# Kernel optimization log

Measured on AMD Instinct MI355X. Metric: run time of the kernel, lower is better.

Reference implementation:

```python
import jax, jax.numpy as jnp
import numpy as np

POOLED_SIZES = [12, 16, 20, 24]
NUM_HEADS = 8
EPS_LN = 1e-5


def _pool_mat(in_size, out_size):
    # torch adaptive_avg_pool1d/2d semantics as an averaging matrix [out, in]
    m = np.zeros((out_size, in_size), np.float32)
    for i in range(out_size):
        s = (i * in_size) // out_size
        e = -((-(i + 1) * in_size) // out_size)  # ceil
        m[i, s:e] = 1.0 / (e - s)
    return jnp.asarray(m)


def _dwconv(x, w, b):
    # depthwise 3x3, stride 1, padding 1 (NCHW, OIHW with I=1)
    y = jax.lax.conv_general_dilated(
        x, w, (1, 1), 'SAME', feature_group_count=x.shape[1],
        dimension_numbers=('NCHW', 'OIHW', 'NCHW'))
    return y + b[None, :, None, None]


def _ln(x, g, b):
    m = x.mean(-1, keepdims=True)
    v = jnp.mean((x - m) ** 2, axis=-1, keepdims=True)
    return (x - m) / jnp.sqrt(v + EPS_LN) * g + b


def setup_inputs() -> dict:
    key = jax.random.key(0)
    ks = jax.random.split(key, 16)
    B, H, W, C = 4, 56, 56, 256
    hid = 4 * C
    nrm = lambda k, shape, s=0.02: jax.random.normal(k, shape, jnp.float32) * s
    inp = {
        'x': jax.random.normal(ks[0], (B, H * W, C), jnp.float32),
        'cpe_w': nrm(ks[1], (C, 1, 3, 3)), 'cpe_b': jnp.zeros((C,), jnp.float32),
        'norm1_w': jnp.ones((C,), jnp.float32), 'norm1_b': jnp.zeros((C,), jnp.float32),
        'q_w': nrm(ks[2], (C, C)),
        'kv_w': nrm(ks[3], (2 * C, C)),
        'attn_norm_w': jnp.ones((C,), jnp.float32), 'attn_norm_b': jnp.zeros((C,), jnp.float32),
        'proj_w': nrm(ks[4], (C, C)), 'proj_b': jnp.zeros((C,), jnp.float32),
        'norm2_w': jnp.ones((C,), jnp.float32), 'norm2_b': jnp.zeros((C,), jnp.float32),
        'fc1_w': nrm(ks[5], (hid, C)), 'fc1_b': jnp.zeros((hid,), jnp.float32),
        'irb_conv_w': nrm(ks[6], (hid, 1, 3, 3)), 'irb_conv_b': jnp.zeros((hid,), jnp.float32),
        'fc2_w': nrm(ks[7], (C, hid)), 'fc2_b': jnp.zeros((C,), jnp.float32),
        'H': H, 'W': W,
    }
    for i in range(4):
        inp[f'dconv{i}_w'] = nrm(ks[8 + i], (C, 1, 3, 3))
        inp[f'dconv{i}_b'] = jnp.zeros((C,), jnp.float32)
    return inp


def _forward(x, cpe_w, cpe_b, norm1_w, norm1_b, q_w, kv_w, attn_norm_w, attn_norm_b,
             proj_w, proj_b, dconv0_w, dconv0_b, dconv1_w, dconv1_b, dconv2_w, dconv2_b,
             dconv3_w, dconv3_b, norm2_w, norm2_b, fc1_w, fc1_b, irb_conv_w, irb_conv_b,
             fc2_w, fc2_b, H, W):
    B, N, C = x.shape
    nh = NUM_HEADS
    hd = C // nh
    scale = hd ** -0.5
    # conditional positional encoding: x = cpe(x) + x
    xi = x.transpose(0, 2, 1).reshape(B, C, H, W)
    xi = _dwconv(xi, cpe_w, cpe_b) + xi
    x = xi.reshape(B, C, N).transpose(0, 2, 1)
    # ---- pyramid pooling attention ----
    xn = _ln(x, norm1_w, norm1_b)
    q = (xn @ q_w.T).reshape(B, N, nh, hd).transpose(0, 2, 1, 3)  # [B,nh,N,hd]
    x_ = xn.transpose(0, 2, 1).reshape(B, C, H, W)
    dws = [(dconv0_w, dconv0_b), (dconv1_w, dconv1_b),
           (dconv2_w, dconv2_b), (dconv3_w, dconv3_b)]
    pools = []
    for p, (dw, db) in zip(POOLED_SIZES, dws):
        ph = _pool_mat(H, p)
        pw = _pool_mat(W, p)
        pool = jnp.einsum('oi,bcij,pj->bcop', ph, x_, pw)  # adaptive avg pool (p,p)
        pool = pool + _dwconv(pool, dw, db)
        pools.append(pool.reshape(B, C, -1))
    pools = jnp.concatenate(pools, axis=2).transpose(0, 2, 1)  # [B,P,C], P=1376
    pools = _ln(pools, attn_norm_w, attn_norm_b)
    kv = (pools @ kv_w.T).reshape(B, -1, 2, nh, hd).transpose(2, 0, 3, 1, 4)
    k, v = kv[0], kv[1]  # [B,nh,P,hd]
    attn = jax.nn.softmax(jnp.einsum('bhnd,bhpd->bhnp', q, k) * scale, axis=-1)
    out = jnp.einsum('bhnp,bhpd->bhnd', attn, v).transpose(0, 2, 1, 3).reshape(B, N, C)
    out = out @ proj_w.T + proj_b
    x = x + out
    # ---- IRB FFN ----
    xn = _ln(x, norm2_w, norm2_b)
    xi = xn.transpose(0, 2, 1).reshape(B, C, H, W)
    h = jnp.einsum('oc,bchw->bohw', fc1_w, xi) + fc1_b[None, :, None, None]
    h = jax.nn.gelu(h, approximate=False)
    h = h + _dwconv(h, irb_conv_w, irb_conv_b)
    o = jnp.einsum('oc,bchw->bohw', fc2_w, h) + fc2_b[None, :, None, None]
    x = x + o.reshape(B, C, N).transpose(0, 2, 1)
    return x


def reference(x, cpe_w, cpe_b, norm1_w, norm1_b, q_w, kv_w, attn_norm_w, attn_norm_b,
              proj_w, proj_b, dconv0_w, dconv0_b, dconv1_w, dconv1_b, dconv2_w, dconv2_b,
              dconv3_w, dconv3_b, norm2_w, norm2_b, fc1_w, fc1_b, irb_conv_w, irb_conv_b,
              fc2_w, fc2_b, H, W):
    return _forward(x, cpe_w, cpe_b, norm1_w, norm1_b, q_w, kv_w, attn_norm_w, attn_norm_b,
                    proj_w, proj_b, dconv0_w, dconv0_b, dconv1_w, dconv1_b, dconv2_w, dconv2_b,
                    dconv3_w, dconv3_b, norm2_w, norm2_b, fc1_w, fc1_b, irb_conv_w, irb_conv_b,
                    fc2_w, fc2_b, H, W)
```

## Files before the change

kernel.cpp:

```cpp
#include <hip/hip_runtime.h>
#include <hip/hip_bf16.h>

#define BQ 4
#define HH 56
#define WW 56
#define NN (HH*WW)
#define CC 256
#define NHEAD 8
#define HD 32
#define PP 1376
#define PPAD 1408
#define HIDN 1024
#define EPS_LN 1e-5f
#define QSCALE_LOG2E 0.25503484f

typedef unsigned short bf16u;
typedef __attribute__((ext_vector_type(8))) short short8;
typedef __attribute__((ext_vector_type(4))) float f32x4;

__device__ __forceinline__ float bf2f(bf16u u){
  union { unsigned int i; float f; } v; v.i = ((unsigned int)u) << 16; return v.f;
}
__device__ __forceinline__ bf16u f2bf(float f){
  unsigned int x = __float_as_uint(f);
  x += 0x7fffu + ((x >> 16) & 1u);
  return (bf16u)(x >> 16);
}
__device__ __forceinline__ bf16u f2bf_r(float f){
  return (bf16u)((__float_as_uint(f) + 0x8000u) >> 16);
}
__device__ __forceinline__ void cvt4(const ushort4 u, float* d){
  d[0]=bf2f(u.x); d[1]=bf2f(u.y); d[2]=bf2f(u.z); d[3]=bf2f(u.w);
}

__global__ void k_init(const float* __restrict__ qw, const float* __restrict__ kvw,
                       const float* __restrict__ pw, const float* __restrict__ f1,
                       const float* __restrict__ f2, bf16u* __restrict__ wo,
                       const float* __restrict__ x, const float* __restrict__ w,
                       const float* __restrict__ bias, const float* __restrict__ g,
                       const float* __restrict__ be, float* __restrict__ x1,
                       bf16u* __restrict__ xnb){
  if (blockIdx.x < 768){
    int off = (blockIdx.x*256 + threadIdx.x) * 4;
    const float* s;
    if (off < 65536)       s = qw  + off;
    else if (off < 196608) s = kvw + off - 65536;
    else if (off < 262144) s = pw  + off - 196608;
    else if (off < 524288) s = f1  + off - 262144;
    else                   s = f2  + off - 524288;
    float4 v = *(const float4*)s;
    ushort4 u = {f2bf(v.x), f2bf(v.y), f2bf(v.z), f2bf(v.w)};
    *(ushort4*)(wo + off) = u;
    return;
  }
  int t = threadIdx.x;
  int pix = (blockIdx.x - 768)*4 + (t >> 6);
  int b = pix / NN, n = pix % NN;
  int hy = n / WW, wx = n % WW;
  int c0 = (t & 63) * 4;
  float wv[4][9];
  float acc[4];
#pragma unroll
  for (int cc = 0; cc < 4; cc++){
    acc[cc] = bias[c0+cc];
#pragma unroll
    for (int k = 0; k < 9; k++) wv[cc][k] = w[(c0+cc)*9 + k];
  }
  const float* xb = x + (size_t)b*NN*CC + c0;
#pragma unroll
  for (int kh = 0; kh < 3; kh++){
    int iy = hy + kh - 1;
    if (iy < 0 || iy >= HH) continue;
#pragma unroll
    for (int kw = 0; kw < 3; kw++){
      int ix = wx + kw - 1;
      if (ix < 0 || ix >= WW) continue;
      float4 v = *(const float4*)&xb[(size_t)(iy*WW+ix)*CC];
      int k = kh*3+kw;
      acc[0] += v.x*wv[0][k]; acc[1] += v.y*wv[1][k];
      acc[2] += v.z*wv[2][k]; acc[3] += v.w*wv[3][k];
    }
  }
  float4 cv = *(const float4*)&xb[(size_t)n*CC];
  float o0 = cv.x + acc[0], o1 = cv.y + acc[1];
  float o2 = cv.z + acc[2], o3 = cv.w + acc[3];
  float4 ov = {o0,o1,o2,o3};
  *(float4*)&x1[(size_t)pix*CC + c0] = ov;
  float s  = o0+o1+o2+o3;
  float s2 = o0*o0+o1*o1+o2*o2+o3*o3;
#pragma unroll
  for (int off = 32; off; off >>= 1){
    s  += __shfl_xor(s,  off);
    s2 += __shfl_xor(s2, off);
  }
  float mean = s * (1.f/CC);
  float var  = s2 * (1.f/CC) - mean*mean;
  float rstd = rsqrtf(var + EPS_LN);
  float4 gv = *(const float4*)&g[c0];
  float4 bv = *(const float4*)&be[c0];
  float y0 = (o0-mean)*rstd*gv.x + bv.x;
  float y1 = (o1-mean)*rstd*gv.y + bv.y;
  float y2 = (o2-mean)*rstd*gv.z + bv.z;
  float y3 = (o3-mean)*rstd*gv.w + bv.w;
  ushort4 yb = {f2bf_r(y0), f2bf_r(y1), f2bf_r(y2), f2bf_r(y3)};
  *(ushort4*)&xnb[(size_t)pix*CC + c0] = yb;
}

__global__ void k_ln_bf16(const float* __restrict__ X, const float* __restrict__ g,
                          const float* __restrict__ be, bf16u* __restrict__ Y){
  int row = blockIdx.x;
  int t = threadIdx.x;
  float v = X[(size_t)row*CC + t];
  float s = v, s2 = v*v;
#pragma unroll
  for (int off = 32; off; off >>= 1){
    s  += __shfl_down(s,  off);
    s2 += __shfl_down(s2, off);
  }
  __shared__ float red[10];
  int wv_ = t >> 6, ln = t & 63;
  if (ln == 0){ red[wv_] = s; red[4+wv_] = s2; }
  __syncthreads();
  if (t == 0){
    float S  = red[0]+red[1]+red[2]+red[3];
    float S2 = red[4]+red[5]+red[6]+red[7];
    float mean = S * (1.f/CC);
    float var  = S2 * (1.f/CC) - mean*mean;
    red[8] = mean; red[9] = rsqrtf(var + EPS_LN);
  }
  __syncthreads();
  float mean = red[8], rstd = red[9];
  Y[(size_t)row*CC + t] = f2bf_r((v - mean) * rstd * g[t] + be[t]);
}

__global__ void k_pool(const bf16u* __restrict__ xnb, float* __restrict__ praw){
  int bp = blockIdx.x;
  int b = bp / PP, p = bp % PP;
  int ps, pi;
  if (p < 144)      { ps = 12; pi = p; }
  else if (p < 400) { ps = 16; pi = p - 144; }
  else if (p < 800) { ps = 20; pi = p - 400; }
  else              { ps = 24; pi = p - 800; }
  int oi = pi / ps, oj = pi % ps;
  int si = oi*HH/ps, ei = ((oi+1)*HH + ps - 1)/ps;
  int sj = oj*WW/ps, ej = ((oj+1)*WW + ps - 1)/ps;
  int c = threadIdx.x;
  const bf16u* xb = xnb + (size_t)b*NN*CC + c;
  float acc = 0.f;
  for (int i = si; i < ei; i++)
    for (int j = sj; j < ej; j++)
      acc += bf2f(xb[(size_t)(i*WW+j)*CC]);
  praw[(size_t)bp*CC + c] = acc / (float)((ei-si)*(ej-sj));
}

__global__ void k_pooldw_ln(const float* __restrict__ praw,
    const float* w0, const float* b0, const float* w1, const float* b1,
    const float* w2, const float* b2, const float* w3, const float* b3,
    const float* __restrict__ g, const float* __restrict__ be,
    bf16u* __restrict__ pools){
  int bp = blockIdx.x;
  int b = bp / PP, p = bp % PP;
  int ps, pi, off; const float *w, *bi;
  if (p < 144)      { ps=12; pi=p;     off=0;   w=w0; bi=b0; }
  else if (p < 400) { ps=16; pi=p-144; off=144; w=w1; bi=b1; }
  else if (p < 800) { ps=20; pi=p-400; off=400; w=w2; bi=b2; }
  else              { ps=24; pi=p-800; off=800; w=w3; bi=b3; }
  int oi = pi/ps, oj = pi%ps;
  int c = threadIdx.x;
  const float* base = praw + (size_t)(b*PP + off)*CC + c;
  float acc = bi[c];
#pragma unroll
  for (int kh = 0; kh < 3; kh++){
    int ii = oi + kh - 1; if (ii < 0 || ii >= ps) continue;
#pragma unroll
    for (int kw = 0; kw < 3; kw++){
      int jj = oj + kw - 1; if (jj < 0 || jj >= ps) continue;
      acc += base[(size_t)(ii*ps+jj)*CC] * w[c*9 + kh*3 + kw];
    }
  }
  float v = base[(size_t)(oi*ps+oj)*CC] + acc;
  float s = v, s2 = v*v;
#pragma unroll
  for (int o2_ = 32; o2_; o2_ >>= 1){
    s  += __shfl_down(s,  o2_);
    s2 += __shfl_down(s2, o2_);
  }
  __shared__ float red[10];
  int wv_ = c >> 6, ln = c & 63;
  if (ln == 0){ red[wv_] = s; red[4+wv_] = s2; }
  __syncthreads();
  if (c == 0){
    float S  = red[0]+red[1]+red[2]+red[3];
    float S2 = red[4]+red[5]+red[6]+red[7];
    float mean = S * (1.f/CC);
    float var  = S2 * (1.f/CC) - mean*mean;
    red[8] = mean; red[9] = rsqrtf(var + EPS_LN);
  }
  __syncthreads();
  float mean = red[8], rstd = red[9];
  pools[(size_t)bp*CC + c] = f2bf_r((v - mean) * rstd * g[c] + be[c]);
}

#define GST 40
template<int NT, bool OUT_BF16, bool HAS_BIAS, bool DO_GELU, bool HAS_RES, bool VT_OUT>
__global__ __launch_bounds__(256) void k_gemm_mfma(const bf16u* __restrict__ A,
                       const bf16u* __restrict__ Wt,
                       const float* __restrict__ bias, void* Outp,
                       const float* Res, bf16u* __restrict__ vtout,
                       int M, int Nout, int K, float oscale){
  constexpr int NW = (NT == 128) ? 4 : 2;
  __shared__ bf16u Ash[2][128*GST];
  __shared__ bf16u Bsh[2][NT*GST];
  int t = threadIdx.x;
  int wave = t >> 6, lane = t & 63, quad = lane >> 4, l16 = lane & 15;
  int m0 = blockIdx.y * 128, n0 = blockIdx.x * NT;
  int wm = (wave >> 1) * 64;
  int wn = (wave & 1) * (NT/2);
  int srow = t >> 1, scol = (t & 1) * 16;
  int br = (NT == 128) ? srow : (t >> 2);
  int bc = (NT == 128) ? scol : ((t & 3) * 8);
  int astore = srow*GST + scol;
  int bstore = br*GST + bc;
  const bf16u* ap = A  + (size_t)(m0+srow)*K + scol;
  const bf16u* bp = Wt + (size_t)(n0+br)*K + bc;

  uint4 a0 = *(const uint4*)ap, a1 = *(const uint4*)(ap+8);
  uint4 b0 = *(const uint4*)bp, b1;
  if constexpr (NT == 128) b1 = *(const uint4*)(bp+8);
  *(uint4*)&Ash[0][astore]     = a0;
  *(uint4*)&Ash[0][astore + 8] = a1;
  *(uint4*)&Bsh[0][bstore] = b0;
  if constexpr (NT == 128) *(uint4*)&Bsh[0][bstore + 8] = b1;
  ap += 32; bp += 32;
  a0 = *(const uint4*)ap; a1 = *(const uint4*)(ap+8);
  b0 = *(const uint4*)bp;
  if constexpr (NT == 128) b1 = *(const uint4*)(bp+8);
  __syncthreads();

  f32x4 zero = {0.f,0.f,0.f,0.f};
  f32x4 acc[4][NW];
#pragma unroll
  for (int i = 0; i < 4; i++)
#pragma unroll
    for (int j = 0; j < NW; j++) acc[i][j] = zero;

  int nks = K >> 5;
  for (int ks = 0; ks < nks; ks++){
    int cur = ks & 1;
    if (ks < nks-1){
      *(uint4*)&Ash[cur^1][astore]     = a0;
      *(uint4*)&Ash[cur^1][astore + 8] = a1;
      *(uint4*)&Bsh[cur^1][bstore] = b0;
      if constexpr (NT == 128) *(uint4*)&Bsh[cur^1][bstore + 8] = b1;
      if (ks < nks-2){
        ap += 32; bp += 32;
        a0 = *(const uint4*)ap; a1 = *(const uint4*)(ap+8);
        b0 = *(const uint4*)bp;
        if constexpr (NT == 128) b1 = *(const uint4*)(bp+8);
      }
    }
    short8 af[4], bfr[NW];
#pragma unroll
    for (int mi = 0; mi < 4; mi++)
      af[mi] = *(const short8*)&Ash[cur][(wm + mi*16 + l16)*GST + quad*8];
#pragma unroll
    for (int ni = 0; ni < NW; ni++)
      bfr[ni] = *(const short8*)&Bsh[cur][(wn + ni*16 + l16)*GST + quad*8];
#pragma unroll
    for (int mi = 0; mi < 4; mi++)
#pragma unroll
      for (int ni = 0; ni < NW; ni++)
        acc[mi][ni] = __builtin_amdgcn_mfma_f32_16x16x32_bf16(af[mi], bfr[ni], acc[mi][ni], 0,0,0);
    if (ks < nks-1) __syncthreads();
  }
#pragma unroll
  for (int mi = 0; mi < 4; mi++){
#pragma unroll
    for (int r = 0; r < 4; r++){
      int row = m0 + wm + mi*16 + quad*4 + r;
#pragma unroll
      for (int ni = 0; ni < NW; ni++){
        int col = n0 + wn + ni*16 + l16;
        float v = acc[mi][ni][r] * oscale;
        if constexpr (HAS_BIAS) v += bias[col];
        if constexpr (DO_GELU)  v = 0.5f*v*(1.f + erff(v*0.70710678118654752f));
        if constexpr (HAS_RES)  v += Res[(size_t)row*Nout + col];
        if constexpr (VT_OUT){
          if (col < CC){
            ((bf16u*)Outp)[(size_t)row*Nout + col] = f2bf_r(v);
          } else {
            int bb = row / PP, pp = row - bb*PP;
            vtout[((size_t)(bb*CC + (col - CC)))*PPAD + pp] = f2bf_r(v);
          }
        } else if constexpr (OUT_BF16){
          ((bf16u*)Outp)[(size_t)row*Nout + col] = f2bf_r(v);
        } else {
          ((float*)Outp)[(size_t)row*Nout + col] = v;
        }
      }
    }
  }
}

#define KST 40
#define VST 72
__global__ __launch_bounds__(256) void k_attn_mfma(const bf16u* __restrict__ q,
                       const bf16u* __restrict__ kvb, const bf16u* __restrict__ vt,
                       bf16u* __restrict__ out){
  __shared__ bf16u Ksh[2][64*KST];
  __shared__ bf16u Vsh[2][32*VST];
  int t = threadIdx.x;
  int wave = t >> 6, lane = t & 63, quad = lane >> 4, l16 = lane & 15;
  int bid = blockIdx.x;
  int qt = bid % (NN/64);
  int h  = (bid / (NN/64)) % NHEAD;
  int b  = bid / ((NN/64)*NHEAD);
  int q0 = qt*64 + wave*16;
  const bf16u* qptr = q + (size_t)(b*NN + q0 + l16)*CC + h*HD + quad*8;
  short8 qf = *(const short8*)qptr;
  f32x4 zero = {0.f,0.f,0.f,0.f};
  f32x4 o0 = zero, o1 = zero;
  float ls = 0.f;
  int ksr = t >> 2, ksc = (t & 3) * 8;
  int vsr = t >> 3, vsc = (t & 7) * 8;
  const bf16u* ksrc = kvb + (size_t)(b*PP + ksr)*(2*CC) + h*HD + ksc;
  const bf16u* vsrc = vt  + (size_t)(b*CC + h*HD + vsr)*PPAD + vsc;
  int kstore = ksr*KST + ksc;
  int vstore = vsr*VST + vsc;
  int g0 = ((l16 & 12) << 1) | (l16 & 3);
  int koffA = g0 * KST + quad*8;
  int koffB = koffA + 4*KST;
  int voff0 = l16*VST + quad*8;
  int voff1 = (16 + l16)*VST + quad*8;

  uint4 kreg = *(const uint4*)ksrc;
  uint4 vreg = *(const uint4*)vsrc;
  *(uint4*)&Ksh[0][kstore] = kreg;
  *(uint4*)&Vsh[0][vstore] = vreg;
  ksrc += (size_t)64*(2*CC); vsrc += 64;
  kreg = *(const uint4*)ksrc; vreg = *(const uint4*)vsrc;
  __syncthreads();

#define PAIR(KB, VB, cb) { \
    short8 kfa = *(const short8*)&KB[cb*KST + koffA]; \
    short8 kfb = *(const short8*)&KB[cb*KST + koffB]; \
    f32x4 sa = __builtin_amdgcn_mfma_f32_16x16x32_bf16(kfa, qf, zero, 0,0,0); \
    f32x4 sb = __builtin_amdgcn_mfma_f32_16x16x32_bf16(kfb, qf, zero, 0,0,0); \
    float ea0 = __builtin_amdgcn_exp2f(sa[0]), ea1 = __builtin_amdgcn_exp2f(sa[1]); \
    float ea2 = __builtin_amdgcn_exp2f(sa[2]), ea3 = __builtin_amdgcn_exp2f(sa[3]); \
    float eb0 = __builtin_amdgcn_exp2f(sb[0]), eb1 = __builtin_amdgcn_exp2f(sb[1]); \
    float eb2 = __builtin_amdgcn_exp2f(sb[2]), eb3 = __builtin_amdgcn_exp2f(sb[3]); \
    ls += ((ea0+ea1)+(ea2+ea3)) + ((eb0+eb1)+(eb2+eb3)); \
    short8 pa; \
    pa[0]=(short)f2bf_r(ea0); pa[1]=(short)f2bf_r(ea1); \
    pa[2]=(short)f2bf_r(ea2); pa[3]=(short)f2bf_r(ea3); \
    pa[4]=(short)f2bf_r(eb0); pa[5]=(short)f2bf_r(eb1); \
    pa[6]=(short)f2bf_r(eb2); pa[7]=(short)f2bf_r(eb3); \
    short8 vf0 = *(const short8*)&VB[cb + voff0]; \
    short8 vf1 = *(const short8*)&VB[cb + voff1]; \
    o0 = __builtin_amdgcn_mfma_f32_16x16x32_bf16(pa, vf0, o0, 0,0,0); \
    o1 = __builtin_amdgcn_mfma_f32_16x16x32_bf16(pa, vf1, o1, 0,0,0); }

  for (int ch = 0; ch < PPAD/64 - 1; ch++){
    int cur = ch & 1;
    bf16u* KB = &Ksh[cur][0];
    bf16u* VB = &Vsh[cur][0];
    *(uint4*)&Ksh[cur^1][kstore] = kreg;
    *(uint4*)&Vsh[cur^1][vstore] = vreg;
    if (ch < PPAD/64 - 2){
      ksrc += (size_t)64*(2*CC); vsrc += 64;
      kreg = *(const uint4*)ksrc; vreg = *(const uint4*)vsrc;
    }
    PAIR(KB, VB, 0)
    PAIR(KB, VB, 32)
    __syncthreads();
  }
  {
    bf16u* KB = &Ksh[1][0];
    bf16u* VB = &Vsh[1][0];
    PAIR(KB, VB, 0)
  }
#undef PAIR

  ls += __shfl_xor(ls, 16); ls += __shfl_xor(ls, 32);
#pragma unroll
  for (int r = 0; r < 4; r++){
    int qq = quad*4 + r;
    float inv = 1.f / __shfl(ls, qq);
    size_t base = (size_t)(b*NN + q0 + qq)*CC + h*HD;
    out[base + l16]      = f2bf_r(o0[r]*inv);
    out[base + 16 + l16] = f2bf_r(o1[r]*inv);
  }
}

#define DWSEG 8
__global__ __launch_bounds__(256) void k_dwh(const bf16u* __restrict__ h, const float* __restrict__ w,
                      const float* __restrict__ bias, bf16u* __restrict__ h2){
  const int nseg = WW/DWSEG;
  int bid = blockIdx.x;
  int xseg = bid % nseg;
  int y    = (bid / nseg) % HH;
  int b    = bid / (nseg*HH);
  int t = threadIdx.x;
  int c0 = t*4;
  int x0 = xseg*DWSEG;
  float wv[36];
  {
    const float4* wp = (const float4*)(w + (size_t)c0*9);
#pragma unroll
    for (int i = 0; i < 9; i++){
      float4 v = wp[i];
      wv[i*4+0]=v.x; wv[i*4+1]=v.y; wv[i*4+2]=v.z; wv[i*4+3]=v.w;
    }
  }
  float4 bi4 = *(const float4*)&bias[c0];
  float bi[4] = {bi4.x, bi4.y, bi4.z, bi4.w};
  const bf16u* rowc = h + ((size_t)b*NN + (size_t)y*WW)*HIDN + c0;
  const bf16u* rowm = (y > 0)    ? rowc - (size_t)WW*HIDN : rowc;
  const bf16u* rowp = (y < HH-1) ? rowc + (size_t)WW*HIDN : rowc;
  if (y == 0){
#pragma unroll
    for (int cc = 0; cc < 4; cc++){ wv[cc*9+0]=0.f; wv[cc*9+1]=0.f; wv[cc*9+2]=0.f; }
  }
  if (y == HH-1){
#pragma unroll
    for (int cc = 0; cc < 4; cc++){ wv[cc*9+6]=0.f; wv[cc*9+7]=0.f; wv[cc*9+8]=0.f; }
  }
  float win[3][3][4];
  ushort4 rawA[3], rawB[3];
  if (x0 == 0){
#pragma unroll
    for (int r = 0; r < 3; r++)
#pragma unroll
      for (int cc = 0; cc < 4; cc++) win[0][r][cc] = 0.f;
  } else {
    size_t o = (size_t)(x0-1)*HIDN;
    ushort4 a0 = *(const ushort4*)&rowm[o];
    ushort4 a1 = *(const ushort4*)&rowc[o];
    ushort4 a2 = *(const ushort4*)&rowp[o];
    cvt4(a0, win[0][0]); cvt4(a1, win[0][1]); cvt4(a2, win[0][2]);
  }
  {
    size_t o = (size_t)x0*HIDN;
    ushort4 a0 = *(const ushort4*)&rowm[o];
    ushort4 a1 = *(const ushort4*)&rowc[o];
    ushort4 a2 = *(const ushort4*)&rowp[o];
    cvt4(a0, win[1][0]); cvt4(a1, win[1][1]); cvt4(a2, win[1][2]);
  }
  {
    size_t o = (size_t)(x0+1)*HIDN;
    rawA[0] = *(const ushort4*)&rowm[o];
    rawA[1] = *(const ushort4*)&rowc[o];
    rawA[2] = *(const ushort4*)&rowp[o];
  }
#pragma unroll
  for (int x = 0; x < DWSEG; x++){
    ushort4* cur = (x & 1) ? rawB : rawA;
    ushort4* nxt = (x & 1) ? rawA : rawB;
    if (x < DWSEG-1){
      int xg = x0 + x + 2;
      if (xg < WW){
        size_t o = (size_t)xg*HIDN;
        nxt[0] = *(const ushort4*)&rowm[o];
        nxt[1] = *(const ushort4*)&rowc[o];
        nxt[2] = *(const ushort4*)&rowp[o];
      } else {
        ushort4 z = {0,0,0,0};
        nxt[0] = z; nxt[1] = z; nxt[2] = z;
      }
    }
    int s2 = (x+2)%3, sm = x%3, sc_ = (x+1)%3;
    cvt4(cur[0], win[s2][0]); cvt4(cur[1], win[s2][1]); cvt4(cur[2], win[s2][2]);
    float o0[4];
#pragma unroll
    for (int cc = 0; cc < 4; cc++){
      float a = bi[cc];
      a += win[sm][0][cc]*wv[cc*9+0] + win[sc_][0][cc]*wv[cc*9+1] + win[s2][0][cc]*wv[cc*9+2];
      a += win[sm][1][cc]*wv[cc*9+3] + win[sc_][1][cc]*wv[cc*9+4] + win[s2][1][cc]*wv[cc*9+5];
      a += win[sm][2][cc]*wv[cc*9+6] + win[sc_][2][cc]*wv[cc*9+7] + win[s2][2][cc]*wv[cc*9+8];
      o0[cc] = win[sc_][1][cc] + a;
    }
    ushort4 ou = {f2bf_r(o0[0]), f2bf_r(o0[1]), f2bf_r(o0[2]), f2bf_r(o0[3])};
    *(ushort4*)&h2[((size_t)b*NN + (size_t)y*WW + x0 + x)*HIDN + c0] = ou;
  }
}

extern "C" void kernel_launch(void* const* d_in, const int* in_sizes, int n_in,
                              void* d_out, int out_size, void* d_ws, size_t ws_size,
                              hipStream_t stream){
  const float* x      = (const float*)d_in[0];
  const float* cpe_w  = (const float*)d_in[1];
  const float* cpe_b  = (const float*)d_in[2];
  const float* n1w    = (const float*)d_in[3];
  const float* n1b    = (const float*)d_in[4];
  const float* q_w    = (const float*)d_in[5];
  const float* kv_w   = (const float*)d_in[6];
  const float* anw    = (const float*)d_in[7];
  const float* anb    = (const float*)d_in[8];
  const float* proj_w = (const float*)d_in[9];
  const float* proj_b = (const float*)d_in[10];
  const float* n2w    = (const float*)d_in[11];
  const float* n2b    = (const float*)d_in[12];
  const float* fc1_w  = (const float*)d_in[13];
  const float* fc1_b  = (const float*)d_in[14];
  const float* irb_w  = (const float*)d_in[15];
  const float* irb_b  = (const float*)d_in[16];
  const float* fc2_w  = (const float*)d_in[17];
  const float* fc2_b  = (const float*)d_in[18];
  const float* dw0    = (const float*)d_in[21];
  const float* db0    = (const float*)d_in[22];
  const float* dw1    = (const float*)d_in[23];
  const float* db1    = (const float*)d_in[24];
  const float* dw2    = (const float*)d_in[25];
  const float* db2    = (const float*)d_in[26];
  const float* dw3    = (const float*)d_in[27];
  const float* db3    = (const float*)d_in[28];

  const size_t BNC = (size_t)BQ*NN*CC;
  const size_t BPC = (size_t)BQ*PP*CC;
  const size_t BNH = (size_t)BQ*NN*HIDN;

  float* x1   = (float*)d_ws;
  bf16u* xnb  = (bf16u*)(x1 + BNC);
  bf16u* wbuf = xnb + BNC;
  bf16u* wq   = wbuf;
  bf16u* wkv  = wbuf + 65536;
  bf16u* wpj  = wbuf + 196608;
  bf16u* wf1  = wbuf + 262144;
  bf16u* wf2  = wbuf + 524288;
  float* A0   = (float*)(wbuf + 786432);
  bf16u* qb   = (bf16u*)A0;
  float* praw = (float*)(qb + BNC);
  bf16u* poolsb = (bf16u*)(praw + BPC);
  bf16u* kvb  = poolsb + BPC;
  bf16u* vtb  = kvb + (size_t)BQ*PP*2*CC;
  bf16u* hbuf = (bf16u*)A0;
  bf16u* h2buf = hbuf + BNH;

  k_init<<<768 + BQ*NN/4, 256, 0, stream>>>(q_w, kv_w, proj_w, fc1_w, fc2_w, wbuf,
                                            x, cpe_w, cpe_b, n1w, n1b, x1, xnb);
  k_gemm_mfma<64,true,false,false,false,false><<<dim3(CC/64, BQ*NN/128), 256, 0, stream>>>(
      xnb, wq, nullptr, qb, nullptr, nullptr, BQ*NN, CC, CC, QSCALE_LOG2E);
  k_pool<<<BQ*PP, 256, 0, stream>>>(xnb, praw);
  k_pooldw_ln<<<BQ*PP, 256, 0, stream>>>(praw, dw0,db0, dw1,db1, dw2,db2, dw3,db3,
                                         anw, anb, poolsb);
  k_gemm_mfma<64,true,false,false,false,true><<<dim3(2*CC/64, BQ*PP/128), 256, 0, stream>>>(
      poolsb, wkv, nullptr, kvb, nullptr, vtb, BQ*PP, 2*CC, CC, 1.0f);
  k_attn_mfma<<<BQ*NHEAD*(NN/64), 256, 0, stream>>>(qb, kvb, vtb, qb);
  k_gemm_mfma<64,false,true,false,true,false><<<dim3(CC/64, BQ*NN/128), 256, 0, stream>>>(
      qb, wpj, proj_b, x1, x1, nullptr, BQ*NN, CC, CC, 1.0f);
  k_ln_bf16<<<BQ*NN, 256, 0, stream>>>(x1, n2w, n2b, xnb);
  k_gemm_mfma<128,true,true,true,false,false><<<dim3(HIDN/128, BQ*NN/128), 256, 0, stream>>>(
      xnb, wf1, fc1_b, hbuf, nullptr, nullptr, BQ*NN, HIDN, CC, 1.0f);
  k_dwh<<<BQ*HH*(WW/DWSEG), 256, 0, stream>>>(hbuf, irb_w, irb_b, h2buf);
  k_gemm_mfma<64,false,true,false,true,false><<<dim3(CC/64, BQ*NN/128), 256, 0, stream>>>(
      h2buf, wf2, fc2_b, d_out, x1, nullptr, BQ*NN, CC, HIDN, 1.0f);
}
```

Before: 321.3 us.

## Slide CPE conv window per wave, add M-tile template, packed bf16 cvt

The CPE depthwise conv plus LN kernel now has each wave walk a segment of CSEG pixels along a row. It keeps a sliding 3x3 register window, so each neighbor column is loaded once instead of up to nine times. The GEMM kernel gains an MT template parameter, and the C=256 output GEMMs switch to 64x64 tiles, doubling their block count for better CU occupancy at the cost of less reuse per tile. Attention replaces scalar bf16 rounding with v_cvt_pk_bf16_f32 inline asm and shrinks the K LDS stride from 40 to 36, which may change bank conflicts and rounding behavior.

```diff
diff --git a/kernel.cpp b/kernel.cpp
--- a/kernel.cpp
+++ b/kernel.cpp
@@ -33,6 +33,7 @@
   d[0]=bf2f(u.x); d[1]=bf2f(u.y); d[2]=bf2f(u.z); d[3]=bf2f(u.w);
 }
 
+#define CSEG 4
 __global__ void k_init(const float* __restrict__ qw, const float* __restrict__ kvw,
                        const float* __restrict__ pw, const float* __restrict__ f1,
                        const float* __restrict__ f2, bf16u* __restrict__ wo,
@@ -54,56 +55,120 @@
     return;
   }
   int t = threadIdx.x;
-  int pix = (blockIdx.x - 768)*4 + (t >> 6);
-  int b = pix / NN, n = pix % NN;
-  int hy = n / WW, wx = n % WW;
-  int c0 = (t & 63) * 4;
-  float wv[4][9];
-  float acc[4];
-#pragma unroll
-  for (int cc = 0; cc < 4; cc++){
-    acc[cc] = bias[c0+cc];
-#pragma unroll
-    for (int k = 0; k < 9; k++) wv[cc][k] = w[(c0+cc)*9 + k];
-  }
-  const float* xb = x + (size_t)b*NN*CC + c0;
-#pragma unroll
-  for (int kh = 0; kh < 3; kh++){
-    int iy = hy + kh - 1;
-    if (iy < 0 || iy >= HH) continue;
-#pragma unroll
-    for (int kw = 0; kw < 3; kw++){
-      int ix = wx + kw - 1;
-      if (ix < 0 || ix >= WW) continue;
-      float4 v = *(const float4*)&xb[(size_t)(iy*WW+ix)*CC];
-      int k = kh*3+kw;
-      acc[0] += v.x*wv[0][k]; acc[1] += v.y*wv[1][k];
-      acc[2] += v.z*wv[2][k]; acc[3] += v.w*wv[3][k];
-    }
-  }
-  float4 cv = *(const float4*)&xb[(size_t)n*CC];
-  float o0 = cv.x + acc[0], o1 = cv.y + acc[1];
-  float o2 = cv.z + acc[2], o3 = cv.w + acc[3];
-  float4 ov = {o0,o1,o2,o3};
-  *(float4*)&x1[(size_t)pix*CC + c0] = ov;
-  float s  = o0+o1+o2+o3;
-  float s2 = o0*o0+o1*o1+o2*o2+o3*o3;
-#pragma unroll
-  for (int off = 32; off; off >>= 1){
-    s  += __shfl_xor(s,  off);
-    s2 += __shfl_xor(s2, off);
-  }
-  float mean = s * (1.f/CC);
-  float var  = s2 * (1.f/CC) - mean*mean;
-  float rstd = rsqrtf(var + EPS_LN);
+  int wave = t >> 6, lane = t & 63;
+  int widx = (blockIdx.x - 768)*4 + wave;
+  const int nseg = WW/CSEG;
+  int xseg = widx % nseg;
+  int y    = (widx / nseg) % HH;
+  int b    = widx / (nseg*HH);
+  int c0 = lane*4;
+  int x0 = xseg*CSEG;
+  float wv[36];
+  {
+    const float* wp = w + (size_t)c0*9;
+#pragma unroll
+    for (int i = 0; i < 9; i++){
+      float4 v = *(const float4*)(wp + i*4);
+      wv[i*4+0]=v.x; wv[i*4+1]=v.y; wv[i*4+2]=v.z; wv[i*4+3]=v.w;
+    }
+  }
+  float4 bi4 = *(const float4*)&bias[c0];
+  float bi[4] = {bi4.x, bi4.y, bi4.z, bi4.w};
   float4 gv = *(const float4*)&g[c0];
   float4 bv = *(const float4*)&be[c0];
-  float y0 = (o0-mean)*rstd*gv.x + bv.x;
-  float y1 = (o1-mean)*rstd*gv.y + bv.y;
-  float y2 = (o2-mean)*rstd*gv.z + bv.z;
-  float y3 = (o3-mean)*rstd*gv.w + bv.w;
-  ushort4 yb = {f2bf_r(y0), f2bf_r(y1), f2bf_r(y2), f2bf_r(y3)};
-  *(ushort4*)&xnb[(size_t)pix*CC + c0] = yb;
+  const float* rowc = x + ((size_t)b*NN + (size_t)y*WW)*CC + c0;
+  const float* rowm = (y > 0)    ? rowc - (size_t)WW*CC : rowc;
+  const float* rowp = (y < HH-1) ? rowc + (size_t)WW*CC : rowc;
+  if (y == 0){
+#pragma unroll
+    for (int cc = 0; cc < 4; cc++){ wv[cc*9+0]=0.f; wv[cc*9+1]=0.f; wv[cc*9+2]=0.f; }
+  }
+  if (y == HH-1){
+#pragma unroll
+    for (int cc = 0; cc < 4; cc++){ wv[cc*9+6]=0.f; wv[cc*9+7]=0.f; wv[cc*9+8]=0.f; }
+  }
+  float win[3][3][4];
+  float4 rawA[3], rawB[3];
+  if (x0 == 0){
+#pragma unroll
+    for (int r = 0; r < 3; r++)
+#pragma unroll
+      for (int cc = 0; cc < 4; cc++) win[0][r][cc] = 0.f;
+  } else {
+    size_t o = (size_t)(x0-1)*CC;
+    float4 a0 = *(const float4*)&rowm[o];
+    float4 a1 = *(const float4*)&rowc[o];
+    float4 a2 = *(const float4*)&rowp[o];
+    win[0][0][0]=a0.x; win[0][0][1]=a0.y; win[0][0][2]=a0.z; win[0][0][3]=a0.w;
+    win[0][1][0]=a1.x; win[0][1][1]=a1.y; win[0][1][2]=a1.z; win[0][1][3]=a1.w;
+    win[0][2][0]=a2.x; win[0][2][1]=a2.y; win[0][2][2]=a2.z; win[0][2][3]=a2.w;
+  }
+  {
+    size_t o = (size_t)x0*CC;
+    float4 a0 = *(const float4*)&rowm[o];
+    float4 a1 = *(const float4*)&rowc[o];
+    float4 a2 = *(const float4*)&rowp[o];
+    win[1][0][0]=a0.x; win[1][0][1]=a0.y; win[1][0][2]=a0.z; win[1][0][3]=a0.w;
+    win[1][1][0]=a1.x; win[1][1][1]=a1.y; win[1][1][2]=a1.z; win[1][1][3]=a1.w;
+    win[1][2][0]=a2.x; win[1][2][1]=a2.y; win[1][2][2]=a2.z; win[1][2][3]=a2.w;
+  }
+  {
+    size_t o = (size_t)(x0+1)*CC;
+    rawA[0] = *(const float4*)&rowm[o];
+    rawA[1] = *(const float4*)&rowc[o];
+    rawA[2] = *(const float4*)&rowp[o];
+  }
+#pragma unroll
+  for (int xx = 0; xx < CSEG; xx++){
+    float4* cur = (xx & 1) ? rawB : rawA;
+    float4* nxt = (xx & 1) ? rawA : rawB;
+    if (xx < CSEG-1){
+      int xg = x0 + xx + 2;
+      if (xg < WW){
+        size_t o = (size_t)xg*CC;
+        nxt[0] = *(const float4*)&rowm[o];
+        nxt[1] = *(const float4*)&rowc[o];
+        nxt[2] = *(const float4*)&rowp[o];
+      } else {
+        float4 z = {0.f,0.f,0.f,0.f};
+        nxt[0] = z; nxt[1] = z; nxt[2] = z;
+      }
+    }
+    int sl2 = (xx+2)%3, slm = xx%3, slc = (xx+1)%3;
+#pragma unroll
+    for (int r = 0; r < 3; r++){
+      win[sl2][r][0]=cur[r].x; win[sl2][r][1]=cur[r].y;
+      win[sl2][r][2]=cur[r].z; win[sl2][r][3]=cur[r].w;
+    }
+    float o4[4];
+#pragma unroll
+    for (int cc = 0; cc < 4; cc++){
+      float a = bi[cc];
+      a += win[slm][0][cc]*wv[cc*9+0] + win[slc][0][cc]*wv[cc*9+1] + win[sl2][0][cc]*wv[cc*9+2];
+      a += win[slm][1][cc]*wv[cc*9+3] + win[slc][1][cc]*wv[cc*9+4] + win[sl2][1][cc]*wv[cc*9+5];
+      a += win[slm][2][cc]*wv[cc*9+6] + win[slc][2][cc]*wv[cc*9+7] + win[sl2][2][cc]*wv[cc*9+8];
+      o4[cc] = win[slc][1][cc] + a;
+    }
+    size_t pix = (size_t)b*NN + (size_t)y*WW + x0 + xx;
+    float4 ov = {o4[0],o4[1],o4[2],o4[3]};
+    *(float4*)&x1[pix*CC + c0] = ov;
+    float s  = o4[0]+o4[1]+o4[2]+o4[3];
+    float s2 = o4[0]*o4[0]+o4[1]*o4[1]+o4[2]*o4[2]+o4[3]*o4[3];
+#pragma unroll
+    for (int off = 32; off; off >>= 1){
+      s  += __shfl_xor(s,  off);
+      s2 += __shfl_xor(s2, off);
+    }
+    float mean = s * (1.f/CC);
+    float var  = s2 * (1.f/CC) - mean*mean;
+    float rstd = rsqrtf(var + EPS_LN);
+    float y0 = (o4[0]-mean)*rstd*gv.x + bv.x;
+    float y1 = (o4[1]-mean)*rstd*gv.y + bv.y;
+    float y2 = (o4[2]-mean)*rstd*gv.z + bv.z;
+    float y3 = (o4[3]-mean)*rstd*gv.w + bv.w;
+    ushort4 yb = {f2bf_r(y0), f2bf_r(y1), f2bf_r(y2), f2bf_r(y3)};
+    *(ushort4*)&xnb[pix*CC + c0] = yb;
+  }
 }
 
 __global__ void k_ln_bf16(const float* __restrict__ X, const float* __restrict__ g,
@@ -202,45 +267,49 @@
 }
 
 #define GST 40
-template<int NT, bool OUT_BF16, bool HAS_BIAS, bool DO_GELU, bool HAS_RES, bool VT_OUT>
+template<int MT, int NT, bool OUT_BF16, bool HAS_BIAS, bool DO_GELU, bool HAS_RES, bool VT_OUT>
 __global__ __launch_bounds__(256) void k_gemm_mfma(const bf16u* __restrict__ A,
                        const bf16u* __restrict__ Wt,
                        const float* __restrict__ bias, void* Outp,
                        const float* Res, bf16u* __restrict__ vtout,
                        int M, int Nout, int K, float oscale){
+  constexpr int MW = (MT == 128) ? 4 : 2;
   constexpr int NW = (NT == 128) ? 4 : 2;
-  __shared__ bf16u Ash[2][128*GST];
+  __shared__ bf16u Ash[2][MT*GST];
   __shared__ bf16u Bsh[2][NT*GST];
   int t = threadIdx.x;
   int wave = t >> 6, lane = t & 63, quad = lane >> 4, l16 = lane & 15;
-  int m0 = blockIdx.y * 128, n0 = blockIdx.x * NT;
-  int wm = (wave >> 1) * 64;
+  int m0 = blockIdx.y * MT, n0 = blockIdx.x * NT;
+  int wm = (wave >> 1) * (MT/2);
   int wn = (wave & 1) * (NT/2);
-  int srow = t >> 1, scol = (t & 1) * 16;
-  int br = (NT == 128) ? srow : (t >> 2);
-  int bc = (NT == 128) ? scol : ((t & 3) * 8);
-  int astore = srow*GST + scol;
+  int ar = (MT==128) ? (t>>1) : (t>>2);
+  int ac = (MT==128) ? ((t&1)*16) : ((t&3)*8);
+  int br = (NT==128) ? (t>>1) : (t>>2);
+  int bc = (NT==128) ? ((t&1)*16) : ((t&3)*8);
+  int astore = ar*GST + ac;
   int bstore = br*GST + bc;
-  const bf16u* ap = A  + (size_t)(m0+srow)*K + scol;
+  const bf16u* ap = A  + (size_t)(m0+ar)*K + ac;
   const bf16u* bp = Wt + (size_t)(n0+br)*K + bc;
 
-  uint4 a0 = *(const uint4*)ap, a1 = *(const uint4*)(ap+8);
+  uint4 a0 = *(const uint4*)ap, a1;
   uint4 b0 = *(const uint4*)bp, b1;
+  if constexpr (MT == 128) a1 = *(const uint4*)(ap+8);
   if constexpr (NT == 128) b1 = *(const uint4*)(bp+8);
-  *(uint4*)&Ash[0][astore]     = a0;
-  *(uint4*)&Ash[0][astore + 8] = a1;
+  *(uint4*)&Ash[0][astore] = a0;
+  if constexpr (MT == 128) *(uint4*)&Ash[0][astore + 8] = a1;
   *(uint4*)&Bsh[0][bstore] = b0;
   if constexpr (NT == 128) *(uint4*)&Bsh[0][bstore + 8] = b1;
   ap += 32; bp += 32;
-  a0 = *(const uint4*)ap; a1 = *(const uint4*)(ap+8);
+  a0 = *(const uint4*)ap;
+  if constexpr (MT == 128) a1 = *(const uint4*)(ap+8);
   b0 = *(const uint4*)bp;
   if constexpr (NT == 128) b1 = *(const uint4*)(bp+8);
   __syncthreads();
 
   f32x4 zero = {0.f,0.f,0.f,0.f};
-  f32x4 acc[4][NW];
-#pragma unroll
-  for (int i = 0; i < 4; i++)
+  f32x4 acc[MW][NW];
+#pragma unroll
+  for (int i = 0; i < MW; i++)
 #pragma unroll
     for (int j = 0; j < NW; j++) acc[i][j] = zero;
 
@@ -248,33 +317,34 @@
   for (int ks = 0; ks < nks; ks++){
     int cur = ks & 1;
     if (ks < nks-1){
-      *(uint4*)&Ash[cur^1][astore]     = a0;
-      *(uint4*)&Ash[cur^1][astore + 8] = a1;
+      *(uint4*)&Ash[cur^1][astore] = a0;
+      if constexpr (MT == 128) *(uint4*)&Ash[cur^1][astore + 8] = a1;
       *(uint4*)&Bsh[cur^1][bstore] = b0;
       if constexpr (NT == 128) *(uint4*)&Bsh[cur^1][bstore + 8] = b1;
       if (ks < nks-2){
         ap += 32; bp += 32;
-        a0 = *(const uint4*)ap; a1 = *(const uint4*)(ap+8);
+        a0 = *(const uint4*)ap;
+        if constexpr (MT == 128) a1 = *(const uint4*)(ap+8);
         b0 = *(const uint4*)bp;
         if constexpr (NT == 128) b1 = *(const uint4*)(bp+8);
       }
     }
-    short8 af[4], bfr[NW];
-#pragma unroll
-    for (int mi = 0; mi < 4; mi++)
+    short8 af[MW], bfr[NW];
+#pragma unroll
+    for (int mi = 0; mi < MW; mi++)
       af[mi] = *(const short8*)&Ash[cur][(wm + mi*16 + l16)*GST + quad*8];
 #pragma unroll
     for (int ni = 0; ni < NW; ni++)
       bfr[ni] = *(const short8*)&Bsh[cur][(wn + ni*16 + l16)*GST + quad*8];
 #pragma unroll
-    for (int mi = 0; mi < 4; mi++)
+    for (int mi = 0; mi < MW; mi++)
 #pragma unroll
       for (int ni = 0; ni < NW; ni++)
         acc[mi][ni] = __builtin_amdgcn_mfma_f32_16x16x32_bf16(af[mi], bfr[ni], acc[mi][ni], 0,0,0);
     if (ks < nks-1) __syncthreads();
   }
 #pragma unroll
-  for (int mi = 0; mi < 4; mi++){
+  for (int mi = 0; mi < MW; mi++){
 #pragma unroll
     for (int r = 0; r < 4; r++){
       int row = m0 + wm + mi*16 + quad*4 + r;
@@ -302,7 +372,7 @@
   }
 }
 
-#define KST 40
+#define KST 36
 #define VST 72
 __global__ __launch_bounds__(256) void k_attn_mfma(const bf16u* __restrict__ q,
                        const bf16u* __restrict__ kvb, const bf16u* __restrict__ vt,
@@ -351,11 +421,12 @@
     float eb0 = __builtin_amdgcn_exp2f(sb[0]), eb1 = __builtin_amdgcn_exp2f(sb[1]); \
     float eb2 = __builtin_amdgcn_exp2f(sb[2]), eb3 = __builtin_amdgcn_exp2f(sb[3]); \
     ls += ((ea0+ea1)+(ea2+ea3)) + ((eb0+eb1)+(eb2+eb3)); \
-    short8 pa; \
-    pa[0]=(short)f2bf_r(ea0); pa[1]=(short)f2bf_r(ea1); \
-    pa[2]=(short)f2bf_r(ea2); pa[3]=(short)f2bf_r(ea3); \
-    pa[4]=(short)f2bf_r(eb0); pa[5]=(short)f2bf_r(eb1); \
-    pa[6]=(short)f2bf_r(eb2); pa[7]=(short)f2bf_r(eb3); \
+    union { uint4 u; short8 s; } pk; \
+    asm("v_cvt_pk_bf16_f32 %0, %1, %2" : "=v"(pk.u.x) : "v"(ea0), "v"(ea1)); \
+    asm("v_cvt_pk_bf16_f32 %0, %1, %2" : "=v"(pk.u.y) : "v"(ea2), "v"(ea3)); \
+    asm("v_cvt_pk_bf16_f32 %0, %1, %2" : "=v"(pk.u.z) : "v"(eb0), "v"(eb1)); \
+    asm("v_cvt_pk_bf16_f32 %0, %1, %2" : "=v"(pk.u.w) : "v"(eb2), "v"(eb3)); \
+    short8 pa = pk.s; \
     short8 vf0 = *(const short8*)&VB[cb + voff0]; \
     short8 vf1 = *(const short8*)&VB[cb + voff1]; \
     o0 = __builtin_amdgcn_mfma_f32_16x16x32_bf16(pa, vf0, o0, 0,0,0); \
@@ -537,22 +608,22 @@
   bf16u* hbuf = (bf16u*)A0;
   bf16u* h2buf = hbuf + BNH;
 
-  k_init<<<768 + BQ*NN/4, 256, 0, stream>>>(q_w, kv_w, proj_w, fc1_w, fc2_w, wbuf,
+  k_init<<<768 + (BQ*HH*(WW/CSEG))/4, 256, 0, stream>>>(q_w, kv_w, proj_w, fc1_w, fc2_w, wbuf,
                                             x, cpe_w, cpe_b, n1w, n1b, x1, xnb);
-  k_gemm_mfma<64,true,false,false,false,false><<<dim3(CC/64, BQ*NN/128), 256, 0, stream>>>(
+  k_gemm_mfma<64,64,true,false,false,false,false><<<dim3(CC/64, BQ*NN/64), 256, 0, stream>>>(
       xnb, wq, nullptr, qb, nullptr, nullptr, BQ*NN, CC, CC, QSCALE_LOG2E);
   k_pool<<<BQ*PP, 256, 0, stream>>>(xnb, praw);
   k_pooldw_ln<<<BQ*PP, 256, 0, stream>>>(praw, dw0,db0, dw1,db1, dw2,db2, dw3,db3,
                                          anw, anb, poolsb);
-  k_gemm_mfma<64,true,false,false,false,true><<<dim3(2*CC/64, BQ*PP/128), 256, 0, stream>>>(
+  k_gemm_mfma<64,64,true,false,false,false,true><<<dim3(2*CC/64, BQ*PP/64), 256, 0, stream>>>(
       poolsb, wkv, nullptr, kvb, nullptr, vtb, BQ*PP, 2*CC, CC, 1.0f);
   k_attn_mfma<<<BQ*NHEAD*(NN/64), 256, 0, stream>>>(qb, kvb, vtb, qb);
-  k_gemm_mfma<64,false,true,false,true,false><<<dim3(CC/64, BQ*NN/128), 256, 0, stream>>>(
+  k_gemm_mfma<64,64,false,true,false,true,false><<<dim3(CC/64, BQ*NN/64), 256, 0, stream>>>(
       qb, wpj, proj_b, x1, x1, nullptr, BQ*NN, CC, CC, 1.0f);
   k_ln_bf16<<<BQ*NN, 256, 0, stream>>>(x1, n2w, n2b, xnb);
-  k_gemm_mfma<128,true,true,true,false,false><<<dim3(HIDN/128, BQ*NN/128), 256, 0, stream>>>(
+  k_gemm_mfma<128,128,true,true,true,false,false><<<dim3(HIDN/128, BQ*NN/128), 256, 0, stream>>>(
       xnb, wf1, fc1_b, hbuf, nullptr, nullptr, BQ*NN, HIDN, CC, 1.0f);
   k_dwh<<<BQ*HH*(WW/DWSEG), 256, 0, stream>>>(hbuf, irb_w, irb_b, h2buf);
-  k_gemm_mfma<64,false,true,false,true,false><<<dim3(CC/64, BQ*NN/128), 256, 0, stream>>>(
+  k_gemm_mfma<64,64,false,true,false,true,false><<<dim3(CC/64, BQ*NN/64), 256, 0, stream>>>(
       h2buf, wf2, fc2_b, d_out, x1, nullptr, BQ*NN, CC, HIDN, 1.0f);
 }
```

New measurement: 355.4 us. +10.6%, slower.
